# Performance work log

Measured on AMD Instinct MI355X. Metric: run time of the kernel, lower is better.

The kernel has to match this reference:

```python
import jax, jax.numpy as jnp
import numpy as np

VOCAB = 50000; EMB = 256; H = 256; HID = 2 * H  # bidirectional output dim
B = 64; L = 512
NTAGS = 3; C = NTAGS + 2; START = C - 2; STOP = C - 1
IMPOSSIBLE = -1e4


def setup_inputs() -> dict:
    key = jax.random.key(0)
    ks = jax.random.split(key, 11)
    s = 0.05
    xs = jax.random.randint(ks[0], (B, L), 1, VOCAB)  # >0 so masks all True
    emb = jax.random.normal(ks[1], (VOCAB, EMB), jnp.float32) * s
    Wih0 = jax.random.normal(ks[2], (2, 4 * H, EMB), jnp.float32) * s
    Whh0 = jax.random.normal(ks[3], (2, 4 * H, H), jnp.float32) * s
    b0 = jax.random.normal(ks[4], (2, 4 * H), jnp.float32) * s
    WihL = jax.random.normal(ks[5], (3, 2, 4 * H, HID), jnp.float32) * s
    WhhL = jax.random.normal(ks[6], (3, 2, 4 * H, H), jnp.float32) * s
    bL = jax.random.normal(ks[7], (3, 2, 4 * H), jnp.float32) * s
    Wfc = jax.random.normal(ks[8], (C, HID), jnp.float32) * s
    bfc = jnp.zeros((C,), jnp.float32)
    trans = jax.random.normal(ks[9], (C, C), jnp.float32) * 0.1
    trans = trans.at[START, :].set(IMPOSSIBLE).at[:, STOP].set(IMPOSSIBLE)
    return dict(xs=xs, emb=emb, Wih0=Wih0, Whh0=Whh0, b0=b0,
                WihL=WihL, WhhL=WhhL, bL=bL, Wfc=Wfc, bfc=bfc, transitions=trans)


def _lstm_dir(x, Wih, Whh, b, reverse):
    # x: [L, B, E]; PyTorch gate order i, f, g, o; bias b = b_ih + b_hh
    Hh = Whh.shape[1]
    Bb = x.shape[1]

    def step(carry, xt):
        h, c = carry
        g = xt @ Wih.T + h @ Whh.T + b
        i, f, gg, o = jnp.split(g, 4, axis=-1)
        c = jax.nn.sigmoid(f) * c + jax.nn.sigmoid(i) * jnp.tanh(gg)
        h = jax.nn.sigmoid(o) * jnp.tanh(c)
        return (h, c), h

    z = jnp.zeros((Bb, Hh), x.dtype)
    _, hs = jax.lax.scan(step, (z, z), x, reverse=reverse)
    return hs  # [L, B, H]


def _bilstm(xs, emb, Wih0, Whh0, b0, WihL, WhhL, bL):
    x = emb[xs].transpose(1, 0, 2)  # [L, B, E]
    Wihs = [Wih0] + [WihL[i] for i in range(WihL.shape[0])]
    Whhs = [Whh0] + [WhhL[i] for i in range(WhhL.shape[0])]
    bs = [b0] + [bL[i] for i in range(bL.shape[0])]
    for l in range(4):
        fwd = _lstm_dir(x, Wihs[l][0], Whhs[l][0], bs[l][0], False)
        bwd = _lstm_dir(x, Wihs[l][1], Whhs[l][1], bs[l][1], True)
        x = jnp.concatenate([fwd, bwd], axis=-1)  # [L, B, 2H]
    return x.transpose(1, 0, 2)  # [B, L, HID]


def reference(xs, emb, Wih0, Whh0, b0, WihL, WhhL, bL, Wfc, bfc, transitions):
    masks = xs > 0  # [B, L]
    features = _bilstm(xs, emb, Wih0, Whh0, b0, WihL, WhhL, bL)  # [B, L, HID]
    emit = features @ Wfc.T + bfc  # [B, L, C]
    Bb = xs.shape[0]

    # Viterbi decode: transitions[to, from]
    init = jnp.full((Bb, C), IMPOSSIBLE, emit.dtype).at[:, START].set(0.0)

    def vstep(ms, inp):
        e_t, m_t = inp  # [B, C], [B]
        acc = ms[:, None, :] + transitions[None]  # [B, to, from]
        bp = jnp.argmax(acc, axis=-1)             # [B, C]
        best = jnp.max(acc, axis=-1) + e_t
        return jnp.where(m_t[:, None], best, ms), bp

    max_score, bps = jax.lax.scan(vstep, init, (emit.transpose(1, 0, 2), masks.T))
    final = max_score + transitions[STOP]
    best_score = jnp.max(final, axis=-1)   # [B]
    best_tag = jnp.argmax(final, axis=-1)  # [B]

    # Backtrace (all sequences full length since masks all True)
    def bstep(tag, bp):
        prev = jnp.take_along_axis(bp, tag[:, None], axis=1)[:, 0]
        return prev, tag

    tag0, rest = jax.lax.scan(bstep, best_tag, bps[1:], reverse=True)
    tag_seq = jnp.concatenate([tag0[None], rest], axis=0).T  # [B, L]
    return best_score, tag_seq, features, masks
```

## Files before the change

### kernel.cpp

```cpp
#include <hip/hip_runtime.h>
#include <stdint.h>

#define BB 64
#define LL 512
#define EE 256
#define HH 256
#define HID2 512
#define G4 1024
#define MM (LL*BB)
#define CH 128
#define MROWS (CH*BB)
#define IMPOSSIBLE_V (-1e4f)

#define PSTRIDE 1284
#define HSBASE 10272
#define S_FLOATS 15392

__device__ __forceinline__ void agent_store_u64(uint64_t* p, uint64_t v){
  __hip_atomic_store(p, v, __ATOMIC_RELAXED, __HIP_MEMORY_SCOPE_AGENT);
}

__global__ __launch_bounds__(256) void k_embed(const int* __restrict__ xs,
      const float* __restrict__ emb, float* __restrict__ Xt){
  int id = blockIdx.x*256 + threadIdx.x;
  int m  = id & (MM-1);
  int e4 = (id >> 15) << 2;
  int t = m >> 6, b = m & 63;
  int tok = xs[b*LL + t];
  float4 v = *(const float4*)&emb[(size_t)tok*EE + e4];
  Xt[(size_t)(e4+0)*MM + m] = v.x;
  Xt[(size_t)(e4+1)*MM + m] = v.y;
  Xt[(size_t)(e4+2)*MM + m] = v.z;
  Xt[(size_t)(e4+3)*MM + m] = v.w;
}

__global__ __launch_bounds__(256) void k_ingemm(const float* __restrict__ Xt, int KD,
      const float* __restrict__ W, const float* __restrict__ bias,
      float* __restrict__ G, int t0d0, int t0d1){
  __shared__ float As[32*132];
  __shared__ float Bs[32*68];
  const int tid = threadIdx.x;
  const int m0 = blockIdx.x*128, j0 = blockIdx.y*64, dir = blockIdx.z;
  const int t0 = (dir==0) ? t0d0 : t0d1;
  const float* Wd = W + (size_t)dir*G4*KD;
  const float* Xg = Xt + (size_t)t0*BB;
  float acc[8][4];
  #pragma unroll
  for(int i=0;i<8;i++){
    #pragma unroll
    for(int j=0;j<4;j++) acc[i][j]=0.f;
  }
  const int tx = tid & 15, ty = tid >> 4;
  const int kr = tid >> 3, mq = tid & 7;
  const int bj = tid >> 2, bk = (tid & 3)*8;
  for(int kt=0; kt<KD; kt+=32){
    #pragma unroll
    for(int i=0;i<4;i++){
      float4 a = *(const float4*)&Xg[(size_t)(kt+kr)*MM + m0 + mq*16 + i*4];
      *(float4*)&As[kr*132 + mq*16 + i*4] = a;
    }
    {
      const float* wp = &Wd[(size_t)(j0 + bj)*KD + kt + bk];
      float4 w0 = *(const float4*)wp;
      float4 w1 = *(const float4*)(wp+4);
      Bs[(bk+0)*68 + bj] = w0.x;
      Bs[(bk+1)*68 + bj] = w0.y;
      Bs[(bk+2)*68 + bj] = w0.z;
      Bs[(bk+3)*68 + bj] = w0.w;
      Bs[(bk+4)*68 + bj] = w1.x;
      Bs[(bk+5)*68 + bj] = w1.y;
      Bs[(bk+6)*68 + bj] = w1.z;
      Bs[(bk+7)*68 + bj] = w1.w;
    }
    __syncthreads();
    #pragma unroll
    for(int k=0;k<32;k++){
      float bq[4], aq[8];
      *(float4*)bq     = *(const float4*)&Bs[k*68 + tx*4];
      *(float4*)aq     = *(const float4*)&As[k*132 + ty*8];
      *(float4*)(aq+4) = *(const float4*)&As[k*132 + ty*8 + 4];
      #pragma unroll
      for(int i=0;i<8;i++){
        #pragma unroll
        for(int j=0;j<4;j++)
          acc[i][j] += aq[i]*bq[j];
      }
    }
    __syncthreads();
  }
  #pragma unroll
  for(int j=0;j<4;j++){
    int jj = j0 + tx*4 + j;
    float bb_ = bias[dir*G4 + jj];
    float* q = &G[((size_t)dir*G4 + jj)*MROWS + m0 + ty*8];
    float4 v0 = {acc[0][j]+bb_, acc[1][j]+bb_, acc[2][j]+bb_, acc[3][j]+bb_};
    float4 v1 = {acc[4][j]+bb_, acc[5][j]+bb_, acc[6][j]+bb_, acc[7][j]+bb_};
    *(float4*)q = v0;
    *(float4*)(q+4) = v1;
  }
}

__global__ __launch_bounds__(256,1) void k_scan(const float* __restrict__ G,
      const float* __restrict__ Whh, float* __restrict__ Xout,
      float* __restrict__ hbuf, float* __restrict__ cbuf,
      int* __restrict__ flags, int chunk, int sbase, int first){
  __shared__ float S[S_FLOATS];
  const int dir = blockIdx.y, w = blockIdx.x, tid = threadIdx.x;
  const int ug = w >> 2, bg = w & 3;
  const int u0 = ug*16, b0 = bg*16;
  const int ks = tid & 15, rp = tid >> 4;
  const int ul = tid >> 4, bb = tid & 15;
  float Wreg[4][16];
  #pragma unroll
  for(int ri=0;ri<4;ri++){
    const int Rl = rp*4 + ri;
    const float* wsrc = &Whh[((size_t)dir*G4 + (Rl>>4)*256 + u0 + (Rl&15))*HH + ks];
    #pragma unroll
    for(int kk=0;kk<16;kk++) Wreg[ri][kk] = wsrc[kk*16];
  }
  float creg = first ? 0.f : cbuf[((size_t)dir*HH + u0+ul)*BB + b0 + bb];
  if(first){
    for(int i=tid;i<5120;i+=256) S[HSBASE + i] = 0.f;
  }
  __syncthreads();

  int* gflag = &flags[(size_t)(dir*4 + bg)*32];

  for(int it=0; it<CH; it++){
    const int sg = sbase + it;
    const int t  = (dir==0) ? (chunk*CH + it) : (LL-1 - chunk*CH - it);
    const int lt = (dir==0) ? it : (CH-1-it);
    float gp0,gp1,gp2,gp3;
    {
      const float* gb = &G[((size_t)dir*G4 + u0 + ul)*MROWS + (size_t)lt*BB + b0 + bb];
      gp0 = gb[0];
      gp1 = gb[(size_t)256*MROWS];
      gp2 = gb[(size_t)512*MROWS];
      gp3 = gb[(size_t)768*MROWS];
    }
    if(!(first && it==0)){
      if(tid < 4){
        const int4* fp = (const int4*)gflag + tid;
        int spins = 0;
        while(true){
          int4 f;
          asm volatile("global_load_dwordx4 %0, %1, off sc1\n\ts_waitcnt vmcnt(0)"
                       : "=v"(f) : "v"(fp) : "memory");
          if(f.x>=sg && f.y>=sg && f.z>=sg && f.w>=sg) break;
          __builtin_amdgcn_s_sleep(1);
          if(++spins > (1<<22)) break;
        }
      }
      __syncthreads();
      const float4* hb4 = (const float4*)&hbuf[(size_t)((((sg+1)&1)*2 + dir)*4 + bg)*4096];
      float4 h0,h1,h2,h3;
      asm volatile("global_load_dwordx4 %0, %1, off sc1" : "=v"(h0) : "v"(hb4 + 0*256 + tid));
      asm volatile("global_load_dwordx4 %0, %1, off sc1" : "=v"(h1) : "v"(hb4 + 1*256 + tid));
      asm volatile("global_load_dwordx4 %0, %1, off sc1" : "=v"(h2) : "v"(hb4 + 2*256 + tid));
      asm volatile("global_load_dwordx4 %0, %1, off sc1" : "=v"(h3) : "v"(hb4 + 3*256 + tid));
      asm volatile("s_waitcnt vmcnt(0)" ::: "memory");
      __builtin_amdgcn_sched_barrier(0);
      {
        const int i0 = 0*256 + tid, i1 = 1*256 + tid, i2 = 2*256 + tid, i3 = 3*256 + tid;
        *(float4*)&S[HSBASE + (i0>>2)*20 + (i0&3)*4] = h0;
        *(float4*)&S[HSBASE + (i1>>2)*20 + (i1&3)*4] = h1;
        *(float4*)&S[HSBASE + (i2>>2)*20 + (i2&3)*4] = h2;
        *(float4*)&S[HSBASE + (i3>>2)*20 + (i3&3)*4] = h3;
      }
      __syncthreads();
    }
    float acc[4][16];
    #pragma unroll
    for(int ri=0;ri<4;ri++){
      #pragma unroll
      for(int bi=0;bi<16;bi++) acc[ri][bi]=0.f;
    }
    {
      const float* hsb = &S[HSBASE + ks*20];
      #pragma unroll
      for(int kk=0;kk<16;kk++){
        float4 ha  = *(const float4*)&hsb[kk*320 + 0];
        float4 hb_ = *(const float4*)&hsb[kk*320 + 4];
        float4 hc  = *(const float4*)&hsb[kk*320 + 8];
        float4 hd  = *(const float4*)&hsb[kk*320 + 12];
        float hq[16] = {ha.x,ha.y,ha.z,ha.w, hb_.x,hb_.y,hb_.z,hb_.w,
                        hc.x,hc.y,hc.z,hc.w, hd.x,hd.y,hd.z,hd.w};
        #pragma unroll
        for(int ri=0;ri<4;ri++){
          const float wv = Wreg[ri][kk];
          #pragma unroll
          for(int bi=0;bi<16;bi++) acc[ri][bi] += wv*hq[bi];
        }
      }
    }
    if(ks < 8){
      float* pb = &S[(size_t)ks*PSTRIDE + rp*80];
      #pragma unroll
      for(int ri=0;ri<4;ri++){
        #pragma unroll
        for(int bq=0;bq<4;bq++){
          float4 v = {acc[ri][bq*4+0],acc[ri][bq*4+1],acc[ri][bq*4+2],acc[ri][bq*4+3]};
          *(float4*)&pb[ri*20 + bq*4] = v;
        }
      }
    }
    __syncthreads();
    if(ks >= 8){
      float* pb = &S[(size_t)(ks-8)*PSTRIDE + rp*80];
      #pragma unroll
      for(int ri=0;ri<4;ri++){
        #pragma unroll
        for(int bq=0;bq<4;bq++){
          float4 v = *(const float4*)&pb[ri*20 + bq*4];
          v.x += acc[ri][bq*4+0]; v.y += acc[ri][bq*4+1];
          v.z += acc[ri][bq*4+2]; v.w += acc[ri][bq*4+3];
          *(float4*)&pb[ri*20 + bq*4] = v;
        }
      }
    }
    __syncthreads();
    float gs0=gp0, gs1=gp1, gs2=gp2, gs3=gp3;
    {
      const float* pb = &S[ul*20 + bb];
      #pragma unroll
      for(int s=0;s<8;s++){
        gs0 += pb[s*PSTRIDE +   0];
        gs1 += pb[s*PSTRIDE + 320];
        gs2 += pb[s*PSTRIDE + 640];
        gs3 += pb[s*PSTRIDE + 960];
      }
    }
    float si = 1.f/(1.f + expf(-gs0));
    float sf = 1.f/(1.f + expf(-gs1));
    float so = 1.f/(1.f + expf(-gs3));
    creg = sf*creg + si*tanhf(gs2);
    float hv = so*tanhf(creg);
    S[HSBASE + ul*17 + bb] = hv;
    __syncthreads();
    if(tid < 64){
      const int uu = tid>>2, bq = tid&3;
      union { float f[4]; uint64_t u[2]; } hw;
      hw.f[0] = S[HSBASE + uu*17 + bq*4+0];
      hw.f[1] = S[HSBASE + uu*17 + bq*4+1];
      hw.f[2] = S[HSBASE + uu*17 + bq*4+2];
      hw.f[3] = S[HSBASE + uu*17 + bq*4+3];
      uint64_t* hd8 = (uint64_t*)&hbuf[(size_t)(((sg&1)*2 + dir)*4 + bg)*4096]
                      + (size_t)(u0+uu)*8 + bq*2;
      agent_store_u64(hd8,   hw.u[0]);
      agent_store_u64(hd8+1, hw.u[1]);
    }
    asm volatile("s_waitcnt vmcnt(0)" ::: "memory");
    if(tid==0)
      __hip_atomic_store(gflag + ug, sg+1,
                         __ATOMIC_RELAXED, __HIP_MEMORY_SCOPE_AGENT);
    Xout[(size_t)(dir*HH + u0+ul)*MM + (size_t)t*BB + b0 + bb] = hv;
  }
  cbuf[((size_t)dir*HH + u0+ul)*BB + b0 + bb] = creg;
}

__global__ __launch_bounds__(256) void k_emit(const float* __restrict__ Xt,
      const float* __restrict__ Wfc, const float* __restrict__ bfc, float* __restrict__ E){
  __shared__ float Wf[5*512];
  int tid = threadIdx.x;
  for(int i=tid;i<5*512;i+=256) Wf[i] = Wfc[i];
  __syncthreads();
  int m = blockIdx.x*256 + tid;
  float a0=0,a1=0,a2=0,a3=0,a4=0;
  #pragma unroll 4
  for(int k=0;k<512;k++){
    float x = Xt[(size_t)k*MM + m];
    a0 += x*Wf[k]; a1 += x*Wf[512+k]; a2 += x*Wf[1024+k]; a3 += x*Wf[1536+k]; a4 += x*Wf[2048+k];
  }
  float* e = &E[(size_t)m*8];
  e[0]=a0+bfc[0]; e[1]=a1+bfc[1]; e[2]=a2+bfc[2]; e[3]=a3+bfc[3]; e[4]=a4+bfc[4];
}

__global__ __launch_bounds__(256) void k_feat(const float* __restrict__ Xt,
      float* __restrict__ feat){
  __shared__ float T[64][65];
  const int t = blockIdx.y, h0 = blockIdx.x*64;
  const int tid = threadIdx.x;
  const int hr = tid>>2, q = tid&3;
  const float* src = &Xt[(size_t)(h0+hr)*MM + (size_t)t*BB + q*16];
  #pragma unroll
  for(int i=0;i<4;i++){
    float4 v = *(const float4*)&src[i*4];
    T[hr][q*16+i*4+0]=v.x; T[hr][q*16+i*4+1]=v.y;
    T[hr][q*16+i*4+2]=v.z; T[hr][q*16+i*4+3]=v.w;
  }
  __syncthreads();
  float* dst = &feat[((size_t)hr*LL + t)*HID2 + h0 + q*16];
  #pragma unroll
  for(int i=0;i<16;i+=4){
    float4 v = {T[q*16+i+0][hr], T[q*16+i+1][hr], T[q*16+i+2][hr], T[q*16+i+3][hr]};
    *(float4*)&dst[i] = v;
  }
}

__global__ __launch_bounds__(256) void k_mask(float* __restrict__ masks){
  int id = blockIdx.x*256 + threadIdx.x;
  if(id < MM) masks[id] = 1.0f;
}

__global__ __launch_bounds__(64) void k_viterbi(const float* __restrict__ E,
      const float* __restrict__ trans, float* __restrict__ out_score,
      float* __restrict__ out_tags){
  __shared__ uint16_t bps[LL*BB];
  const int b = threadIdx.x;
  float T[25];
  #pragma unroll
  for(int i=0;i<25;i++) T[i] = trans[i];
  float ms[5];
  #pragma unroll
  for(int c=0;c<5;c++) ms[c] = IMPOSSIBLE_V;
  ms[3] = 0.f;
  float4 c0 = *(const float4*)&E[(size_t)b*8];
  float  c4 = E[(size_t)b*8 + 4];
  for(int t=0;t<LL;t++){
    float4 n0 = c0; float n4 = c4;
    if(t < LL-1){
      const float* e = &E[(size_t)((t+1)*BB + b)*8];
      n0 = *(const float4*)e; n4 = e[4];
    }
    float ee[5] = {c0.x, c0.y, c0.z, c0.w, c4};
    float ns[5]; int pack = 0;
    #pragma unroll
    for(int to=0;to<5;to++){
      float best = ms[0] + T[to*5+0]; int bi = 0;
      #pragma unroll
      for(int f=1;f<5;f++){
        float v = ms[f] + T[to*5+f];
        if(v > best){ best = v; bi = f; }
      }
      ns[to] = best + ee[to];
      pack |= bi << (3*to);
    }
    bps[t*BB + b] = (uint16_t)pack;
    #pragma unroll
    for(int c=0;c<5;c++) ms[c] = ns[c];
    c0 = n0; c4 = n4;
  }
  float best = ms[0] + T[4*5+0]; int tag = 0;
  #pragma unroll
  for(int f=1;f<5;f++){
    float v = ms[f] + T[4*5+f];
    if(v > best){ best = v; tag = f; }
  }
  out_score[b] = best;
  out_tags[b*LL + (LL-1)] = (float)tag;
  for(int t=LL-1; t>=1; t--){
    tag = (bps[t*BB + b] >> (3*tag)) & 7;
    out_tags[b*LL + t-1] = (float)tag;
  }
}

extern "C" void kernel_launch(void* const* d_in, const int* in_sizes, int n_in,
                              void* d_out, int out_size, void* d_ws, size_t ws_size,
                              hipStream_t stream){
  const int*   xs    = (const int*)d_in[0];
  const float* emb   = (const float*)d_in[1];
  const float* Wih0  = (const float*)d_in[2];
  const float* Whh0  = (const float*)d_in[3];
  const float* b0    = (const float*)d_in[4];
  const float* WihL  = (const float*)d_in[5];
  const float* WhhL  = (const float*)d_in[6];
  const float* bL    = (const float*)d_in[7];
  const float* Wfc   = (const float*)d_in[8];
  const float* bfc   = (const float*)d_in[9];
  const float* trans = (const float*)d_in[10];

  char* ws = (char*)d_ws;
  int*   flags = (int*)ws;
  float* hbuf  = (float*)(ws + 32768);
  float* cbuf  = (float*)(ws + 32768 + 262144);
  float* Xa    = (float*)(ws + (size_t)(1<<20));
  float* Xb    = (float*)(ws + (size_t)(1<<20) + ((size_t)MM*HID2*4));
  float* G     = (float*)(ws + (size_t)(1<<20) + 2*((size_t)MM*HID2*4));
  float* emitb = G;

  (void)hipMemsetAsync(flags, 0, 8192, stream);
  k_embed<<<8192, 256, 0, stream>>>(xs, emb, Xa);
  float* cur = Xa; float* nxt = Xb;
  for(int l=0;l<4;l++){
    int KD = (l==0) ? 256 : 512;
    const float* Wih = (l==0) ? Wih0 : WihL + (size_t)(l-1)*2*G4*HID2;
    const float* Whh = (l==0) ? Whh0 : WhhL + (size_t)(l-1)*2*G4*HH;
    const float* bb  = (l==0) ? b0   : bL  + (size_t)(l-1)*2*G4;
    for(int chunk=0; chunk<4; chunk++){
      int t0d0 = chunk*CH;
      int t0d1 = (LL-CH) - chunk*CH;
      k_ingemm<<<dim3(MROWS/128, G4/64, 2), 256, 0, stream>>>(cur, KD, Wih, bb, G, t0d0, t0d1);
      k_scan<<<dim3(64, 2), 256, 0, stream>>>(G, Whh, nxt, hbuf, cbuf, flags,
                                              chunk, (l*4+chunk)*CH, chunk==0 ? 1 : 0);
    }
    float* tmp = cur; cur = nxt; nxt = tmp;
  }
  k_emit<<<MM/256, 256, 0, stream>>>(cur, Wfc, bfc, emitb);
  float* out       = (float*)d_out;
  float* out_score = out;
  float* out_tags  = out + 64;
  float* out_feat  = out + 64 + MM;
  float* out_masks = out + 64 + MM + (size_t)MM*HID2;
  k_feat<<<dim3(HID2/64, LL), 256, 0, stream>>>(cur, out_feat);
  k_mask<<<MM/256, 256, 0, stream>>>(out_masks);
  k_viterbi<<<1, 64, 0, stream>>>(emitb, trans, out_score, out_tags);
}
```

Baseline: 12.61 ms.

## Co-locate scan group blocks per XCC and use workgroup-scope L2 atomics for sync

Remaps the recurrent scan grid so the 16 blocks sharing a direction/batch group are strided by 8 in block index, which under round-robin dispatch should land them on the same XCC. A startup handshake reads the XCC id register and checks whether all 16 blocks of a group really share an XCC. If they do, per-step flag polling and h exchange use workgroup-scope atomics on the XCC-local L2 instead of sc1 agent-coherent loads and stores. Otherwise it falls back to the old agent-scope path, with flags spread onto separate cache lines. The aim is lower per-timestep cross-block latency, at the cost of an extra handshake per launch and reliance on dispatch placement and memory-model subtleties.

```diff
diff --git a/kernel.cpp b/kernel.cpp
--- a/kernel.cpp
+++ b/kernel.cpp
@@ -16,9 +16,9 @@
 #define HSBASE 10272
 #define S_FLOATS 15392
 
-__device__ __forceinline__ void agent_store_u64(uint64_t* p, uint64_t v){
-  __hip_atomic_store(p, v, __ATOMIC_RELAXED, __HIP_MEMORY_SCOPE_AGENT);
-}
+#define FL_TST 4096
+#define FL_ACK 4352
+#define FL_VER 4608
 
 __global__ __launch_bounds__(256) void k_embed(const int* __restrict__ xs,
       const float* __restrict__ emb, float* __restrict__ Xt){
@@ -105,11 +105,74 @@
       float* __restrict__ hbuf, float* __restrict__ cbuf,
       int* __restrict__ flags, int chunk, int sbase, int first){
   __shared__ float S[S_FLOATS];
-  const int dir = blockIdx.y, w = blockIdx.x, tid = threadIdx.x;
-  const int ug = w >> 2, bg = w & 3;
+  const int lid = blockIdx.x, tid = threadIdx.x;
+  const int gid = lid & 7, ug = lid >> 3;
+  const int dir = gid >> 2, bg = gid & 3;
   const int u0 = ug*16, b0 = bg*16;
   const int ks = tid & 15, rp = tid >> 4;
   const int ul = tid >> 4, bb = tid & 15;
+
+  int zreg;
+  asm volatile("v_mov_b32 %0, 0" : "=v"(zreg));
+
+  int* gflag = &flags[(size_t)gid*512];
+
+  if(tid==0){
+    int xcc;
+    asm volatile("s_getreg_b32 %0, hwreg(20, 0, 32)" : "=s"(xcc));
+    int* tline = &flags[FL_TST + gid*32];
+    int* aslot = &flags[FL_ACK + gid*32];
+    int* vslot = &flags[FL_VER + (sbase>>7)*8 + gid];
+    int fail = 0;
+    for(int r=0;r<3;r++){
+      const int epoch = (sbase<<3) + r + 1;
+      __hip_atomic_exchange(tline + ug, (epoch<<6)|(xcc&63),
+                            __ATOMIC_RELAXED, __HIP_MEMORY_SCOPE_WORKGROUP);
+      if(ug==0){
+        int ok = 1, x0 = -1;
+        for(int u=0;u<16;u++){
+          int v = 0, spins = 0;
+          while(true){
+            v = __hip_atomic_fetch_add(tline + u, zreg,
+                                       __ATOMIC_RELAXED, __HIP_MEMORY_SCOPE_WORKGROUP);
+            if((v>>6) == epoch) break;
+            __builtin_amdgcn_s_sleep(2);
+            if(++spins > (1<<12)){ ok = 0; break; }
+          }
+          if(!ok) break;
+          if(u==0) x0 = v & 63;
+          else if((v & 63) != x0){ ok = 0; break; }
+        }
+        fail |= !ok;
+        __hip_atomic_exchange(aslot, ok ? epoch : -epoch,
+                              __ATOMIC_RELAXED, __HIP_MEMORY_SCOPE_WORKGROUP);
+      } else {
+        int spins = 0;
+        while(true){
+          int a = __hip_atomic_fetch_add(aslot, zreg,
+                                         __ATOMIC_RELAXED, __HIP_MEMORY_SCOPE_WORKGROUP);
+          if(a == epoch) break;
+          if(a == -epoch){ fail = 1; break; }
+          __builtin_amdgcn_s_sleep(2);
+          if(++spins > (1<<13)){ fail = 1; break; }
+        }
+      }
+    }
+    if(ug==0)
+      __hip_atomic_store(vslot, fail ? 1 : 2, __ATOMIC_RELAXED, __HIP_MEMORY_SCOPE_AGENT);
+    int v = 0, spins = 0;
+    while(true){
+      v = __hip_atomic_load(vslot, __ATOMIC_RELAXED, __HIP_MEMORY_SCOPE_AGENT);
+      if(v) break;
+      __builtin_amdgcn_s_sleep(1);
+      if(++spins > (1<<18)) break;
+    }
+    S[0] = (v == 2) ? 1.f : 0.f;
+  }
+  __syncthreads();
+  const bool localp = (S[0] != 0.f);
+  __syncthreads();
+
   float Wreg[4][16];
   #pragma unroll
   for(int ri=0;ri<4;ri++){
@@ -123,8 +186,6 @@
     for(int i=tid;i<5120;i+=256) S[HSBASE + i] = 0.f;
   }
   __syncthreads();
-
-  int* gflag = &flags[(size_t)(dir*4 + bg)*32];
 
   for(int it=0; it<CH; it++){
     const int sg = sbase + it;
@@ -139,27 +200,45 @@
       gp3 = gb[(size_t)768*MROWS];
     }
     if(!(first && it==0)){
-      if(tid < 4){
-        const int4* fp = (const int4*)gflag + tid;
-        int spins = 0;
-        while(true){
-          int4 f;
-          asm volatile("global_load_dwordx4 %0, %1, off sc1\n\ts_waitcnt vmcnt(0)"
-                       : "=v"(f) : "v"(fp) : "memory");
-          if(f.x>=sg && f.y>=sg && f.z>=sg && f.w>=sg) break;
-          __builtin_amdgcn_s_sleep(1);
-          if(++spins > (1<<22)) break;
-        }
-      }
-      __syncthreads();
       const float4* hb4 = (const float4*)&hbuf[(size_t)((((sg+1)&1)*2 + dir)*4 + bg)*4096];
       float4 h0,h1,h2,h3;
-      asm volatile("global_load_dwordx4 %0, %1, off sc1" : "=v"(h0) : "v"(hb4 + 0*256 + tid));
-      asm volatile("global_load_dwordx4 %0, %1, off sc1" : "=v"(h1) : "v"(hb4 + 1*256 + tid));
-      asm volatile("global_load_dwordx4 %0, %1, off sc1" : "=v"(h2) : "v"(hb4 + 2*256 + tid));
-      asm volatile("global_load_dwordx4 %0, %1, off sc1" : "=v"(h3) : "v"(hb4 + 3*256 + tid));
-      asm volatile("s_waitcnt vmcnt(0)" ::: "memory");
-      __builtin_amdgcn_sched_barrier(0);
+      if(localp){
+        if(tid < 16){
+          int* fp = gflag + tid*32;
+          int spins = 0;
+          while(__hip_atomic_fetch_add(fp, zreg,
+                  __ATOMIC_RELAXED, __HIP_MEMORY_SCOPE_WORKGROUP) < sg){
+            __builtin_amdgcn_s_sleep(1);
+            if(++spins > (1<<18)) break;
+          }
+        }
+        __syncthreads();
+        __builtin_amdgcn_fence(__ATOMIC_ACQUIRE, "agent");
+        h0 = hb4[0*256 + tid];
+        h1 = hb4[1*256 + tid];
+        h2 = hb4[2*256 + tid];
+        h3 = hb4[3*256 + tid];
+      } else {
+        if(tid < 16){
+          const int* fp = gflag + tid*32;
+          int spins = 0;
+          while(true){
+            int f;
+            asm volatile("global_load_dword %0, %1, off sc1\n\ts_waitcnt vmcnt(0)"
+                         : "=v"(f) : "v"(fp) : "memory");
+            if(f >= sg) break;
+            __builtin_amdgcn_s_sleep(1);
+            if(++spins > (1<<20)) break;
+          }
+        }
+        __syncthreads();
+        asm volatile("global_load_dwordx4 %0, %1, off sc1" : "=v"(h0) : "v"(hb4 + 0*256 + tid));
+        asm volatile("global_load_dwordx4 %0, %1, off sc1" : "=v"(h1) : "v"(hb4 + 1*256 + tid));
+        asm volatile("global_load_dwordx4 %0, %1, off sc1" : "=v"(h2) : "v"(hb4 + 2*256 + tid));
+        asm volatile("global_load_dwordx4 %0, %1, off sc1" : "=v"(h3) : "v"(hb4 + 3*256 + tid));
+        asm volatile("s_waitcnt vmcnt(0)" ::: "memory");
+        __builtin_amdgcn_sched_barrier(0);
+      }
       {
         const int i0 = 0*256 + tid, i1 = 1*256 + tid, i2 = 2*256 + tid, i3 = 3*256 + tid;
         *(float4*)&S[HSBASE + (i0>>2)*20 + (i0&3)*4] = h0;
@@ -235,24 +314,23 @@
     float so = 1.f/(1.f + expf(-gs3));
     creg = sf*creg + si*tanhf(gs2);
     float hv = so*tanhf(creg);
-    S[HSBASE + ul*17 + bb] = hv;
+    {
+      float* hp = &hbuf[(size_t)(((sg&1)*2 + dir)*4 + bg)*4096 + (size_t)ug*256 + tid];
+      if(localp)
+        __hip_atomic_exchange((int*)hp, __float_as_int(hv),
+                              __ATOMIC_RELAXED, __HIP_MEMORY_SCOPE_WORKGROUP);
+      else
+        __hip_atomic_store(hp, hv, __ATOMIC_RELAXED, __HIP_MEMORY_SCOPE_AGENT);
+    }
+    asm volatile("s_waitcnt vmcnt(0)" ::: "memory");
     __syncthreads();
-    if(tid < 64){
-      const int uu = tid>>2, bq = tid&3;
-      union { float f[4]; uint64_t u[2]; } hw;
-      hw.f[0] = S[HSBASE + uu*17 + bq*4+0];
-      hw.f[1] = S[HSBASE + uu*17 + bq*4+1];
-      hw.f[2] = S[HSBASE + uu*17 + bq*4+2];
-      hw.f[3] = S[HSBASE + uu*17 + bq*4+3];
-      uint64_t* hd8 = (uint64_t*)&hbuf[(size_t)(((sg&1)*2 + dir)*4 + bg)*4096]
-                      + (size_t)(u0+uu)*8 + bq*2;
-      agent_store_u64(hd8,   hw.u[0]);
-      agent_store_u64(hd8+1, hw.u[1]);
-    }
-    asm volatile("s_waitcnt vmcnt(0)" ::: "memory");
-    if(tid==0)
-      __hip_atomic_store(gflag + ug, sg+1,
-                         __ATOMIC_RELAXED, __HIP_MEMORY_SCOPE_AGENT);
+    if(tid==0){
+      int* fp = gflag + ug*32;
+      if(localp)
+        __hip_atomic_exchange(fp, sg+1, __ATOMIC_RELAXED, __HIP_MEMORY_SCOPE_WORKGROUP);
+      else
+        __hip_atomic_store(fp, sg+1, __ATOMIC_RELAXED, __HIP_MEMORY_SCOPE_AGENT);
+    }
     Xout[(size_t)(dir*HH + u0+ul)*MM + (size_t)t*BB + b0 + bb] = hv;
   }
   cbuf[((size_t)dir*HH + u0+ul)*BB + b0 + bb] = creg;
@@ -378,7 +456,7 @@
   float* G     = (float*)(ws + (size_t)(1<<20) + 2*((size_t)MM*HID2*4));
   float* emitb = G;
 
-  (void)hipMemsetAsync(flags, 0, 8192, stream);
+  (void)hipMemsetAsync(flags, 0, 20480, stream);
   k_embed<<<8192, 256, 0, stream>>>(xs, emb, Xa);
   float* cur = Xa; float* nxt = Xb;
   for(int l=0;l<4;l++){
@@ -390,8 +468,8 @@
       int t0d0 = chunk*CH;
       int t0d1 = (LL-CH) - chunk*CH;
       k_ingemm<<<dim3(MROWS/128, G4/64, 2), 256, 0, stream>>>(cur, KD, Wih, bb, G, t0d0, t0d1);
-      k_scan<<<dim3(64, 2), 256, 0, stream>>>(G, Whh, nxt, hbuf, cbuf, flags,
-                                              chunk, (l*4+chunk)*CH, chunk==0 ? 1 : 0);
+      k_scan<<<dim3(128), 256, 0, stream>>>(G, Whh, nxt, hbuf, cbuf, flags,
+                                            chunk, (l*4+chunk)*CH, chunk==0 ? 1 : 0);
     }
     float* tmp = cur; cur = nxt; nxt = tmp;
   }
```

New measurement: 18.98 ms. 50.5% more time.

## Specialize waves in LSTM scan for publish, poll and output store

Applied to the files above, without the earlier changes.

Restructures the persistent recurrent scan kernel so that the h publish and flag release for step t-1 happen at the start of step t in wave 1. Wave 3 writes the output row for that step as a coalesced float4 store, and only wave 0 polls the flags and loads the remote h tile with 16 loads per thread. This removes one block-wide barrier per step and moves the gate preload after the barrier. The aim is to shorten the critical path between cross-block steps, at the cost of concentrating the h loads on one wave and reusing the partial-sum region of LDS to stage h. The spin timeout is also reduced.

```diff
diff --git a/kernel.cpp b/kernel.cpp
--- a/kernel.cpp
+++ b/kernel.cpp
@@ -110,6 +110,8 @@
   const int u0 = ug*16, b0 = bg*16;
   const int ks = tid & 15, rp = tid >> 4;
   const int ul = tid >> 4, bb = tid & 15;
+  const int wave = tid >> 6;
+
   float Wreg[4][16];
   #pragma unroll
   for(int ri=0;ri<4;ri++){
@@ -130,15 +132,30 @@
     const int sg = sbase + it;
     const int t  = (dir==0) ? (chunk*CH + it) : (LL-1 - chunk*CH - it);
     const int lt = (dir==0) ? it : (CH-1-it);
-    float gp0,gp1,gp2,gp3;
-    {
-      const float* gb = &G[((size_t)dir*G4 + u0 + ul)*MROWS + (size_t)lt*BB + b0 + bb];
-      gp0 = gb[0];
-      gp1 = gb[(size_t)256*MROWS];
-      gp2 = gb[(size_t)512*MROWS];
-      gp3 = gb[(size_t)768*MROWS];
-    }
-    if(!(first && it==0)){
+    if(it > 0){
+      if(wave==1){
+        const int wl = tid - 64, uu = wl>>2, bq = wl&3;
+        union { float f[4]; uint64_t u[2]; } hw;
+        hw.f[0] = S[uu*20 + bq*4 + 0];
+        hw.f[1] = S[uu*20 + bq*4 + 1];
+        hw.f[2] = S[uu*20 + bq*4 + 2];
+        hw.f[3] = S[uu*20 + bq*4 + 3];
+        uint64_t* hd8 = (uint64_t*)&hbuf[(size_t)((((sg-1)&1)*2 + dir)*4 + bg)*4096]
+                        + (size_t)ug*128 + wl*2;
+        agent_store_u64(hd8,   hw.u[0]);
+        agent_store_u64(hd8+1, hw.u[1]);
+        asm volatile("s_waitcnt vmcnt(0)" ::: "memory");
+        if(wl==0)
+          __hip_atomic_store(gflag + ug, sg, __ATOMIC_RELAXED, __HIP_MEMORY_SCOPE_AGENT);
+      } else if(wave==3){
+        const int wl = tid - 192, uu = wl>>2, bq = wl&3;
+        const int tp = (dir==0) ? (chunk*CH + it-1) : (LL-1 - chunk*CH - (it-1));
+        float4 xv = { S[uu*20 + bq*4 + 0], S[uu*20 + bq*4 + 1],
+                      S[uu*20 + bq*4 + 2], S[uu*20 + bq*4 + 3] };
+        *(float4*)&Xout[(size_t)(dir*HH + u0+uu)*MM + (size_t)tp*BB + b0 + bq*4] = xv;
+      }
+    }
+    if((it > 0 || !first) && wave==0){
       if(tid < 4){
         const int4* fp = (const int4*)gflag + tid;
         int spins = 0;
@@ -148,26 +165,31 @@
                        : "=v"(f) : "v"(fp) : "memory");
           if(f.x>=sg && f.y>=sg && f.z>=sg && f.w>=sg) break;
           __builtin_amdgcn_s_sleep(1);
-          if(++spins > (1<<22)) break;
+          if(++spins > (1<<20)) break;
         }
       }
-      __syncthreads();
       const float4* hb4 = (const float4*)&hbuf[(size_t)((((sg+1)&1)*2 + dir)*4 + bg)*4096];
-      float4 h0,h1,h2,h3;
-      asm volatile("global_load_dwordx4 %0, %1, off sc1" : "=v"(h0) : "v"(hb4 + 0*256 + tid));
-      asm volatile("global_load_dwordx4 %0, %1, off sc1" : "=v"(h1) : "v"(hb4 + 1*256 + tid));
-      asm volatile("global_load_dwordx4 %0, %1, off sc1" : "=v"(h2) : "v"(hb4 + 2*256 + tid));
-      asm volatile("global_load_dwordx4 %0, %1, off sc1" : "=v"(h3) : "v"(hb4 + 3*256 + tid));
+      float4 hp[16];
+      #pragma unroll
+      for(int j=0;j<16;j++)
+        asm volatile("global_load_dwordx4 %0, %1, off sc1"
+                     : "=v"(hp[j]) : "v"(hb4 + j*64 + tid));
       asm volatile("s_waitcnt vmcnt(0)" ::: "memory");
       __builtin_amdgcn_sched_barrier(0);
-      {
-        const int i0 = 0*256 + tid, i1 = 1*256 + tid, i2 = 2*256 + tid, i3 = 3*256 + tid;
-        *(float4*)&S[HSBASE + (i0>>2)*20 + (i0&3)*4] = h0;
-        *(float4*)&S[HSBASE + (i1>>2)*20 + (i1&3)*4] = h1;
-        *(float4*)&S[HSBASE + (i2>>2)*20 + (i2&3)*4] = h2;
-        *(float4*)&S[HSBASE + (i3>>2)*20 + (i3&3)*4] = h3;
-      }
-      __syncthreads();
+      #pragma unroll
+      for(int j=0;j<16;j++){
+        const int i4 = j*64 + tid;
+        *(float4*)&S[HSBASE + (i4>>2)*20 + (i4&3)*4] = hp[j];
+      }
+    }
+    __syncthreads();
+    float gp0,gp1,gp2,gp3;
+    {
+      const float* gb = &G[((size_t)dir*G4 + u0 + ul)*MROWS + (size_t)lt*BB + b0 + bb];
+      gp0 = gb[0];
+      gp1 = gb[(size_t)256*MROWS];
+      gp2 = gb[(size_t)512*MROWS];
+      gp3 = gb[(size_t)768*MROWS];
     }
     float acc[4][16];
     #pragma unroll
@@ -235,25 +257,33 @@
     float so = 1.f/(1.f + expf(-gs3));
     creg = sf*creg + si*tanhf(gs2);
     float hv = so*tanhf(creg);
-    S[HSBASE + ul*17 + bb] = hv;
-    __syncthreads();
-    if(tid < 64){
-      const int uu = tid>>2, bq = tid&3;
+    S[ul*20 + bb] = hv;
+    __syncthreads();
+    (void)t;
+  }
+  {
+    const int sgl = sbase + CH - 1;
+    if(wave==1){
+      const int wl = tid - 64, uu = wl>>2, bq = wl&3;
       union { float f[4]; uint64_t u[2]; } hw;
-      hw.f[0] = S[HSBASE + uu*17 + bq*4+0];
-      hw.f[1] = S[HSBASE + uu*17 + bq*4+1];
-      hw.f[2] = S[HSBASE + uu*17 + bq*4+2];
-      hw.f[3] = S[HSBASE + uu*17 + bq*4+3];
-      uint64_t* hd8 = (uint64_t*)&hbuf[(size_t)(((sg&1)*2 + dir)*4 + bg)*4096]
-                      + (size_t)(u0+uu)*8 + bq*2;
+      hw.f[0] = S[uu*20 + bq*4 + 0];
+      hw.f[1] = S[uu*20 + bq*4 + 1];
+      hw.f[2] = S[uu*20 + bq*4 + 2];
+      hw.f[3] = S[uu*20 + bq*4 + 3];
+      uint64_t* hd8 = (uint64_t*)&hbuf[(size_t)(((sgl&1)*2 + dir)*4 + bg)*4096]
+                      + (size_t)ug*128 + wl*2;
       agent_store_u64(hd8,   hw.u[0]);
       agent_store_u64(hd8+1, hw.u[1]);
-    }
-    asm volatile("s_waitcnt vmcnt(0)" ::: "memory");
-    if(tid==0)
-      __hip_atomic_store(gflag + ug, sg+1,
-                         __ATOMIC_RELAXED, __HIP_MEMORY_SCOPE_AGENT);
-    Xout[(size_t)(dir*HH + u0+ul)*MM + (size_t)t*BB + b0 + bb] = hv;
+      asm volatile("s_waitcnt vmcnt(0)" ::: "memory");
+      if(wl==0)
+        __hip_atomic_store(gflag + ug, sgl+1, __ATOMIC_RELAXED, __HIP_MEMORY_SCOPE_AGENT);
+    } else if(wave==3){
+      const int wl = tid - 192, uu = wl>>2, bq = wl&3;
+      const int tl = (dir==0) ? (chunk*CH + CH-1) : (LL-1 - chunk*CH - (CH-1));
+      float4 xv = { S[uu*20 + bq*4 + 0], S[uu*20 + bq*4 + 1],
+                    S[uu*20 + bq*4 + 2], S[uu*20 + bq*4 + 3] };
+      *(float4*)&Xout[(size_t)(dir*HH + u0+uu)*MM + (size_t)tl*BB + b0 + bq*4] = xv;
+    }
   }
   cbuf[((size_t)dir*HH + u0+ul)*BB + b0 + bb] = creg;
 }
```

Result: slower. 13.00 ms (+3.1%).
